# Kernel tuning notes

Measured on AMD Instinct MI355X. Metric: run time of the kernel, lower is better.

Reference implementation:

```python
import jax, jax.numpy as jnp
import numpy as np

B, S, D = 2, 2048, 1024
H, DQK, DV = 16, 64, 64
DECAY = 0.85


def _fractal_weights(seq_len: int, decay: float) -> np.ndarray:
    # Dragon-curve hierarchical weights: earlier (coarser) positions get higher
    # weight; weight decays by `decay` per hierarchy level. Normalized to sum 1,
    # matching DragonCurveGenerator.get_hierarchical_weights semantics.
    idx = np.arange(seq_len)
    level = np.floor(np.log2(idx + 1)).astype(np.int32)
    w = decay ** level.astype(np.float32)
    return (w / w.sum()).astype(np.float32)


def setup_inputs() -> dict:
    key = jax.random.key(0)
    kx, kq, kk, kv, ko = jax.random.split(key, 5)
    s = 1.0 / np.sqrt(D)
    return {
        "x": jax.random.normal(kx, (B, S, D), dtype=jnp.float32),
        "Wq": jax.random.normal(kq, (D, H * DQK), dtype=jnp.float32) * s,
        "Wk": jax.random.normal(kk, (D, H * DQK), dtype=jnp.float32) * s,
        "Wv": jax.random.normal(kv, (D, H * DV), dtype=jnp.float32) * s,
        "Wo": jax.random.normal(ko, (H * DV, D), dtype=jnp.float32) * s,
        "fractal_weights": jnp.asarray(_fractal_weights(S, DECAY)),
    }


def reference(x, Wq, Wk, Wv, Wo, fractal_weights):
    b, s, _ = x.shape
    # Projections (Linear with bias=False); weights stored as (in, out).
    Q = (x @ Wq).reshape(b, s, H, DQK).transpose(0, 2, 1, 3)  # [B,H,S,Dqk]
    K = (x @ Wk).reshape(b, s, H, DQK).transpose(0, 2, 1, 3)
    V = (x @ Wv).reshape(b, s, H, DV).transpose(0, 2, 1, 3)   # [B,H,S,Dv]
    scale = 1.0 / jnp.sqrt(jnp.asarray(DQK, dtype=x.dtype))
    scores = jnp.einsum("bhqd,bhkd->bhqk", Q, K) * scale      # [B,H,S,S]
    # Multiplicative per-key fractal bias applied BEFORE softmax.
    scores = scores * fractal_weights[None, None, None, :]
    attn = jax.nn.softmax(scores, axis=-1)
    out = jnp.einsum("bhqk,bhkd->bhqd", attn, V)               # [B,H,S,Dv]
    out = out.transpose(0, 2, 1, 3).reshape(b, s, H * DV)
    return out @ Wo                                            # [B,S,D]
```

## Files before the change

### kernel.cpp

```cpp
#include <hip/hip_runtime.h>
#include <hip/hip_bf16.h>
#include <stdint.h>

#define B_  2
#define S_  2048
#define D_  1024
#define H_  16
#define DH_ 64

typedef __attribute__((ext_vector_type(8))) __bf16    bf16x8;
typedef __attribute__((ext_vector_type(8))) _Float16  f16x8;
typedef __attribute__((ext_vector_type(4))) _Float16  f16x4;
typedef __attribute__((ext_vector_type(2))) __fp16    fp16x2;
typedef __attribute__((ext_vector_type(4))) float     f32x4;

__device__ inline unsigned short f2bf(float f) {
    union { float f; uint32_t u; } v; v.f = f;
    uint32_t r = (v.u + 0x7fffu + ((v.u >> 16) & 1u)) >> 16;
    return (unsigned short)r;
}

__device__ __forceinline__ void g2l16(const unsigned short* g, unsigned short* l) {
    __builtin_amdgcn_global_load_lds(
        (const __attribute__((address_space(1))) unsigned int*)g,
        (__attribute__((address_space(3))) unsigned int*)l,
        16, 0, 0);
}

__global__ void prep(const float* __restrict__ x, unsigned short* __restrict__ xb,
                     const float* __restrict__ s0, const float* __restrict__ s1,
                     const float* __restrict__ s2, const float* __restrict__ s3,
                     unsigned short* __restrict__ d0, unsigned short* __restrict__ d1,
                     unsigned short* __restrict__ d2, unsigned short* __restrict__ d3)
{
    __shared__ float tile[32][33];
    int bid = blockIdx.x, tid = threadIdx.x;
    if (bid < 4096) {
        int i = (bid * 256 + tid) * 4;
        float4 v = *(const float4*)(x + i);
        ushort4 o;
        o.x = f2bf(v.x); o.y = f2bf(v.y); o.z = f2bf(v.z); o.w = f2bf(v.w);
        *(ushort4*)(xb + i) = o;
    } else {
        int tb = bid - 4096;
        int z = tb >> 10, t = tb & 1023;
        int bx = t & 31, by = t >> 5;
        const float* src; unsigned short* dst;
        switch (z) {
            case 0: src = s0; dst = d0; break;
            case 1: src = s1; dst = d1; break;
            case 2: src = s2; dst = d2; break;
            default: src = s3; dst = d3; break;
        }
        int n0 = bx * 32, k0 = by * 32;
        int tx = tid & 31, ty = tid >> 5;
        for (int j = 0; j < 32; j += 8)
            tile[ty + j][tx] = src[(long)(k0 + ty + j) * 1024 + n0 + tx];
        __syncthreads();
        for (int j = 0; j < 32; j += 8)
            dst[(long)(n0 + ty + j) * 1024 + k0 + tx] = f2bf(tile[tx][ty + j]);
    }
}

__global__ __launch_bounds__(512, 4)
void gemm128(const unsigned short* __restrict__ A, const unsigned short* __restrict__ Bt,
             unsigned short* __restrict__ Qo, unsigned short* __restrict__ Ko,
             unsigned short* __restrict__ Vt,
             const float* __restrict__ fw)
{
    __shared__ __align__(16) unsigned short Smem[2][128 * 64];
    unsigned short* As = &Smem[0][0];
    unsigned short* Bs = &Smem[1][0];
    const int tid  = threadIdx.x;
    const int lane = tid & 63, wid = tid >> 6;
    const int quad = lane >> 4, l15 = lane & 15;
    const int ks   = wid >> 2;
    const int wm   = (wid >> 1) & 1, wn = wid & 1;
    const int lin = blockIdx.y * 24 + blockIdx.x;
    const int xcd = lin & 7, idx = lin >> 3;
    const int bn = (xcd & 1) * 12 + idx % 12;
    const int bm = (xcd >> 1) * 8 + idx / 12;
    const int K = 1024;
    f32x4 acc[4][4] = {};
    const long Abase = (long)bm * 128 * K;
    const long Bbase = (long)bn * 128 * K;

    for (int k0 = 0; k0 < K; k0 += 64) {
        __syncthreads();
#pragma unroll
        for (int i = 0; i < 2; i++) {
            int base = i * 512 + wid * 64;
            int slot = base + lane;
            int row = slot >> 3, cp = slot & 7;
            int c = cp ^ (row & 7);
            g2l16(A + Abase + (long)row * K + k0 + c * 8, &As[base * 8]);
        }
#pragma unroll
        for (int i = 0; i < 2; i++) {
            int base = i * 512 + wid * 64;
            int slot = base + lane;
            int row = slot >> 3, cp = slot & 7;
            int c = cp ^ (row & 7);
            g2l16(Bt + Bbase + (long)row * K + k0 + c * 8, &Bs[base * 8]);
        }
        __syncthreads();
        bf16x8 af[4], bfr[4];
#pragma unroll
        for (int t = 0; t < 4; t++) {
            int ra = wm * 64 + t * 16 + l15;
            af[t]  = *(const bf16x8*)(As + ra * 64 + (((ks * 4 + quad) ^ (l15 & 7))) * 8);
            int rb = wn * 64 + t * 16 + l15;
            bfr[t] = *(const bf16x8*)(Bs + rb * 64 + (((ks * 4 + quad) ^ (l15 & 7))) * 8);
        }
#pragma unroll
        for (int tm = 0; tm < 4; tm++)
#pragma unroll
            for (int tn = 0; tn < 4; tn++)
                acc[tm][tn] = __builtin_amdgcn_mfma_f32_16x16x32_bf16(af[tm], bfr[tn], acc[tm][tn], 0, 0, 0);
    }

    __syncthreads();

    float* ov = (float*)&Smem[0][0];
    const int slot = wm * 2 + wn;
    const float Cq = 0.125f * 1.44269504f;

#pragma unroll
    for (int p = 0; p < 4; p++) {
        if (ks == 1) {
#pragma unroll
            for (int tn = 0; tn < 4; tn++)
#pragma unroll
                for (int r = 0; r < 4; r++)
                    ov[((slot * 16) + quad * 4 + r) * 66 + tn * 16 + l15] = acc[p][tn][r];
        }
        __syncthreads();
        if (ks == 0) {
#pragma unroll
            for (int tn = 0; tn < 4; tn++)
#pragma unroll
                for (int r = 0; r < 4; r++) {
                    float v = acc[p][tn][r] + ov[((slot * 16) + quad * 4 + r) * 66 + tn * 16 + l15];
                    int gm = bm * 128 + wm * 64 + p * 16 + quad * 4 + r;
                    int gn = bn * 128 + wn * 64 + tn * 16 + l15;
                    int b = gm >> 11, s = gm & 2047;
                    if (gn < 1024) {
                        int h = gn >> 6, d = gn & 63;
                        Qo[(((long)(b * H_ + h) * S_ + s) << 6) + d] = f2bf(v * Cq);
                    } else if (gn < 2048) {
                        int g = gn - 1024; int h = g >> 6, d = g & 63;
                        Ko[(((long)(b * H_ + h) * S_ + s) << 6) + d] = f2bf(v * fw[s]);
                    } else {
                        int g = gn - 2048; int h = g >> 6, d = g & 63;
                        union { _Float16 h; unsigned short u; } cv;
                        cv.h = (_Float16)v;
                        int sp = s ^ ((d & 8) ? 4 : 0);
                        Vt[((long)(b * H_ + h) * DH_ + d) * S_ + sp] = cv.u;
                    }
                }
        }
        __syncthreads();
    }
}

__global__ __launch_bounds__(256, 4)
void gemm_wo(const unsigned short* __restrict__ A, const unsigned short* __restrict__ Bt,
             float* __restrict__ Cout)
{
    __shared__ __align__(16) unsigned short As[64 * 64];
    __shared__ __align__(16) unsigned short Bs[64 * 64];
    const int tid  = threadIdx.x;
    const int lane = tid & 63, wid = tid >> 6;
    const int quad = lane >> 4, l15 = lane & 15;
    const int lin = blockIdx.y * 16 + blockIdx.x;
    const int xcd = lin & 7, idx = lin >> 3;
    const int bn = (xcd & 1) * 8 + (idx & 7);
    const int bm = (xcd >> 1) * 16 + (idx >> 3);
    const int K = 1024;
    f32x4 acc[4] = {};
    const long Abase = (long)bm * 64 * K;
    const long Bbase = (long)bn * 64 * K;

    for (int k0 = 0; k0 < K; k0 += 64) {
        __syncthreads();
#pragma unroll
        for (int i = 0; i < 2; i++) {
            int base = i * 256 + wid * 64;
            int slot = base + lane;
            int row = slot >> 3, cp = slot & 7;
            int c = cp ^ (row & 7);
            g2l16(A + Abase + (long)row * K + k0 + c * 8, &As[base * 8]);
        }
#pragma unroll
        for (int i = 0; i < 2; i++) {
            int base = i * 256 + wid * 64;
            int slot = base + lane;
            int row = slot >> 3, cp = slot & 7;
            int c = cp ^ (row & 7);
            g2l16(Bt + Bbase + (long)row * K + k0 + c * 8, &Bs[base * 8]);
        }
        __syncthreads();
#pragma unroll
        for (int ks = 0; ks < 2; ks++) {
            bf16x8 af, bfr[4];
            {
                int ra = wid * 16 + l15;
                af = *(const bf16x8*)(As + ra * 64 + (((ks * 4 + quad) ^ (l15 & 7))) * 8);
            }
#pragma unroll
            for (int tt = 0; tt < 4; tt++) {
                int rb = tt * 16 + l15;
                bfr[tt] = *(const bf16x8*)(Bs + rb * 64 + (((ks * 4 + quad) ^ (l15 & 7))) * 8);
            }
#pragma unroll
            for (int tn = 0; tn < 4; tn++)
                acc[tn] = __builtin_amdgcn_mfma_f32_16x16x32_bf16(af, bfr[tn], acc[tn], 0, 0, 0);
        }
    }

    for (int tn = 0; tn < 4; tn++)
        for (int r = 0; r < 4; r++) {
            int gm = bm * 64 + wid * 16 + quad * 4 + r;
            int gn = bn * 64 + tn * 16 + l15;
            Cout[(long)gm * 1024 + gn] = acc[tn][r];
        }
}

__global__ __launch_bounds__(512, 2)
void attn_kernel(const unsigned short* __restrict__ Q, const unsigned short* __restrict__ Kb,
                 const unsigned short* __restrict__ Vt,
                 unsigned short* __restrict__ O)
{
    __shared__ __align__(16) unsigned short smem[2][2][2][64 * 64];

    const int tid  = threadIdx.x;
    const int lane = tid & 63, wid = tid >> 6;
    const int half = wid >> 2, sw = wid & 3;
    const int quad = lane >> 4, l15 = lane & 15;
    const int lin = blockIdx.y * 8 + blockIdx.x;
    const int xcd = lin & 7, idx = lin >> 3;
    const int bh = xcd * 4 + (idx & 3);
    const int qt = idx >> 2;

    const unsigned short* Kg = Kb + (long)bh * S_ * DH_;
    const unsigned short* Vg = Vt + (long)bh * (long)DH_ * S_;

    bf16x8 qf[4][2];
#pragma unroll
    for (int st = 0; st < 4; st++) {
        const unsigned short* Qp = Q + ((long)bh * S_ + qt * 256 + sw * 64 + st * 16 + l15) * DH_ + quad * 8;
        qf[st][0] = *(const bf16x8*)(Qp);
        qf[st][1] = *(const bf16x8*)(Qp + 32);
    }

    auto issue = [&](int buf, int kt) {
#pragma unroll
        for (int i = 0; i < 2; i++) {
            int base = i * 256 + sw * 64;
            int slot = base + lane;
            int row = slot >> 3, cp = slot & 7;
            int c = cp ^ (row & 7);
            g2l16(Kg + ((long)(kt * 64 + row) * 64 + c * 8), &smem[half][buf][0][base * 8]);
        }
#pragma unroll
        for (int i = 0; i < 2; i++) {
            int base = i * 256 + sw * 64;
            int slot = base + lane;
            int row = slot >> 3, cp = slot & 7;
            int c = cp ^ (row & 7);
            g2l16(Vg + ((long)row * S_ + kt * 64 + c * 8), &smem[half][buf][1][base * 8]);
        }
    };

    f32x4 oacc[4][4] = {};
    f32x4 lacc[4] = {};
    const f16x8 vone = {(_Float16)1.f, (_Float16)1.f, (_Float16)1.f, (_Float16)1.f,
                        (_Float16)1.f, (_Float16)1.f, (_Float16)1.f, (_Float16)1.f};

    const int kt0 = half * 16;
    issue(0, kt0);
    __syncthreads();

    const int hf = (((quad & 1) ^ ((l15 >> 3) & 1))) * 4;

    for (int t = 0; t < 16; t++) {
        const int cur = t & 1;
        if (t + 1 < 16) issue(1 - cur, kt0 + t + 1);

        const unsigned short* Kc = &smem[half][cur][0][0];
        const unsigned short* Vc = &smem[half][cur][1][0];

        f32x4 sacc[4][4] = {};
#pragma unroll
        for (int kc = 0; kc < 4; kc++) {
            int row = kc * 16 + l15;
            bf16x8 k0 = *(const bf16x8*)(Kc + (row * 8 + (quad       ^ (l15 & 7))) * 8);
            bf16x8 k1 = *(const bf16x8*)(Kc + (row * 8 + ((4 + quad) ^ (l15 & 7))) * 8);
#pragma unroll
            for (int st = 0; st < 4; st++) {
                sacc[st][kc] = __builtin_amdgcn_mfma_f32_16x16x32_bf16(k0, qf[st][0], sacc[st][kc], 0, 0, 0);
                sacc[st][kc] = __builtin_amdgcn_mfma_f32_16x16x32_bf16(k1, qf[st][1], sacc[st][kc], 0, 0, 0);
            }
        }

        f16x8 vfr[2][4];
#pragma unroll
        for (int c = 0; c < 2; c++)
#pragma unroll
            for (int dt = 0; dt < 4; dt++) {
                int row = dt * 16 + l15;
                int p0 = (c * 4 +     (quad >> 1)) ^ (l15 & 7);
                int p1 = (c * 4 + 2 + (quad >> 1)) ^ (l15 & 7);
                f16x4 v0 = *(const f16x4*)(Vc + row * 64 + p0 * 8 + hf);
                f16x4 v1 = *(const f16x4*)(Vc + row * 64 + p1 * 8 + hf);
                vfr[c][dt] = __builtin_shufflevector(v0, v1, 0, 1, 2, 3, 4, 5, 6, 7);
            }

        f16x8 pk8[4][2];
#pragma unroll
        for (int st = 0; st < 4; st++)
#pragma unroll
            for (int c = 0; c < 2; c++) {
                union { uint4 u; f16x8 v; } pku;
#pragma unroll
                for (int hh = 0; hh < 2; hh++) {
                    float p0 = __builtin_amdgcn_exp2f(sacc[st][2 * c + hh][0]);
                    float p1 = __builtin_amdgcn_exp2f(sacc[st][2 * c + hh][1]);
                    float p2 = __builtin_amdgcn_exp2f(sacc[st][2 * c + hh][2]);
                    float p3 = __builtin_amdgcn_exp2f(sacc[st][2 * c + hh][3]);
                    union { fp16x2 h2; unsigned int u; } a, b;
                    a.h2 = __builtin_amdgcn_cvt_pkrtz(p0, p1);
                    b.h2 = __builtin_amdgcn_cvt_pkrtz(p2, p3);
                    if (hh == 0) { pku.u.x = a.u; pku.u.y = b.u; }
                    else         { pku.u.z = a.u; pku.u.w = b.u; }
                }
                pk8[st][c] = pku.v;
            }

#pragma unroll
        for (int c = 0; c < 2; c++) {
#pragma unroll
            for (int st = 0; st < 4; st++)
                lacc[st] = __builtin_amdgcn_mfma_f32_16x16x32_f16(pk8[st][c], vone, lacc[st], 0, 0, 0);
#pragma unroll
            for (int dt = 0; dt < 4; dt++)
#pragma unroll
                for (int st = 0; st < 4; st++)
                    oacc[st][dt] = __builtin_amdgcn_mfma_f32_16x16x32_f16(pk8[st][c], vfr[c][dt], oacc[st][dt], 0, 0, 0);
        }

        __syncthreads();
    }

    float* ov = (float*)&smem[0][0][0][0];
    float* lv = ov + 128 * 66;
    int b = bh >> 4, h = bh & 15;

#pragma unroll
    for (int p = 0; p < 2; p++) {
        if (half == 1) {
#pragma unroll
            for (int si = 0; si < 2; si++) {
                int st = 2 * p + si;
#pragma unroll
                for (int dt = 0; dt < 4; dt++)
#pragma unroll
                    for (int r = 0; r < 4; r++) {
                        int qr = sw * 32 + si * 16 + quad * 4 + r;
                        ov[qr * 66 + dt * 16 + l15] = oacc[st][dt][r];
                    }
                if (l15 == 0) {
#pragma unroll
                    for (int r = 0; r < 4; r++)
                        lv[sw * 32 + si * 16 + quad * 4 + r] = lacc[st][r];
                }
            }
        }
        __syncthreads();
        if (half == 0) {
#pragma unroll
            for (int si = 0; si < 2; si++) {
                int st = 2 * p + si;
#pragma unroll
                for (int r = 0; r < 4; r++) {
                    int qr = sw * 32 + si * 16 + quad * 4 + r;
                    float inv = 1.0f / (lacc[st][r] + lv[qr]);
                    int srow = qt * 256 + sw * 64 + st * 16 + quad * 4 + r;
#pragma unroll
                    for (int dt = 0; dt < 4; dt++) {
                        float val = oacc[st][dt][r] + ov[qr * 66 + dt * 16 + l15];
                        O[((long)(b * S_ + srow)) * 1024 + h * DH_ + dt * 16 + l15] = f2bf(val * inv);
                    }
                }
            }
        }
        __syncthreads();
    }
}


extern "C" void kernel_launch(void* const* d_in, const int* in_sizes, int n_in,
                              void* d_out, int out_size, void* d_ws, size_t ws_size,
                              hipStream_t stream)
{
    const float* x  = (const float*)d_in[0];
    const float* Wq = (const float*)d_in[1];
    const float* Wk = (const float*)d_in[2];
    const float* Wv = (const float*)d_in[3];
    const float* Wo = (const float*)d_in[4];
    const float* fw = (const float*)d_in[5];
    float* out = (float*)d_out;

    char* ws = (char*)d_ws;
    unsigned short* xb    = (unsigned short*)(ws);
    unsigned short* WqkvT = (unsigned short*)(ws + 8388608);
    unsigned short* WoT   = (unsigned short*)(ws + 14680064);
    unsigned short* Qb    = (unsigned short*)(ws + 16777216);
    unsigned short* Kb    = (unsigned short*)(ws + 25165824);
    unsigned short* Vt    = (unsigned short*)(ws + 33554432);
    unsigned short* Ob    = xb;

    prep<<<dim3(4096 + 4096), dim3(256), 0, stream>>>(
        x, xb, Wq, Wk, Wv, Wo,
        WqkvT, WqkvT + 1024 * 1024, WqkvT + 2 * 1024 * 1024, WoT);
    gemm128<<<dim3(24, 32), dim3(512), 0, stream>>>(xb, WqkvT, Qb, Kb, Vt, fw);
    attn_kernel<<<dim3(S_ / 256, B_ * H_), dim3(512), 0, stream>>>(Qb, Kb, Vt, Ob);
    gemm_wo<<<dim3(16, 64), dim3(256), 0, stream>>>(Ob, WoT, out);
}
```

Measured before the change: 181.9 us.

## Retile QKV projection GEMM to 256x192 tiles with 16 waves, drop split-K reduction

The QKV projection GEMM moves from 128x128 tiles with a two-way split-K across 8 waves to 256x192 tiles computed by 16 waves, each owning a 64x48 sub-tile over the full K. This removes the shared-memory split-K reduction and its extra barriers in the epilogue, and raises data reuse per loaded tile. The grid shrinks from 768 to 256 blocks of 1024 threads, which is exactly one wave of blocks on 256 CUs but lowers occupancy and latency hiding per CU.

```diff
diff --git a/kernel.cpp b/kernel.cpp
--- a/kernel.cpp
+++ b/kernel.cpp
@@ -62,105 +62,96 @@
     }
 }
 
-__global__ __launch_bounds__(512, 4)
+__global__ __launch_bounds__(1024, 4)
 void gemm128(const unsigned short* __restrict__ A, const unsigned short* __restrict__ Bt,
              unsigned short* __restrict__ Qo, unsigned short* __restrict__ Ko,
              unsigned short* __restrict__ Vt,
              const float* __restrict__ fw)
 {
-    __shared__ __align__(16) unsigned short Smem[2][128 * 64];
-    unsigned short* As = &Smem[0][0];
-    unsigned short* Bs = &Smem[1][0];
+    __shared__ __align__(16) unsigned short As[256 * 64];
+    __shared__ __align__(16) unsigned short Bs[192 * 64];
     const int tid  = threadIdx.x;
     const int lane = tid & 63, wid = tid >> 6;
     const int quad = lane >> 4, l15 = lane & 15;
-    const int ks   = wid >> 2;
-    const int wm   = (wid >> 1) & 1, wn = wid & 1;
-    const int lin = blockIdx.y * 24 + blockIdx.x;
+    const int wr = wid >> 2, wc = wid & 3;
+    const int lin = blockIdx.y * 16 + blockIdx.x;
     const int xcd = lin & 7, idx = lin >> 3;
-    const int bn = (xcd & 1) * 12 + idx % 12;
-    const int bm = (xcd >> 1) * 8 + idx / 12;
+    const int bn = (xcd & 1) * 8 + (idx & 7);
+    const int bm = (xcd >> 1) * 4 + (idx >> 3);
     const int K = 1024;
-    f32x4 acc[4][4] = {};
-    const long Abase = (long)bm * 128 * K;
-    const long Bbase = (long)bn * 128 * K;
+    f32x4 acc[4][3] = {};
+    const long Abase = (long)bm * 256 * K;
+    const long Bbase = (long)bn * 192 * K;
 
     for (int k0 = 0; k0 < K; k0 += 64) {
         __syncthreads();
 #pragma unroll
         for (int i = 0; i < 2; i++) {
-            int base = i * 512 + wid * 64;
+            int base = i * 1024 + wid * 64;
             int slot = base + lane;
             int row = slot >> 3, cp = slot & 7;
             int c = cp ^ (row & 7);
             g2l16(A + Abase + (long)row * K + k0 + c * 8, &As[base * 8]);
         }
-#pragma unroll
-        for (int i = 0; i < 2; i++) {
-            int base = i * 512 + wid * 64;
+        {
+            int base = wid * 64;
             int slot = base + lane;
             int row = slot >> 3, cp = slot & 7;
             int c = cp ^ (row & 7);
             g2l16(Bt + Bbase + (long)row * K + k0 + c * 8, &Bs[base * 8]);
         }
-        __syncthreads();
-        bf16x8 af[4], bfr[4];
-#pragma unroll
-        for (int t = 0; t < 4; t++) {
-            int ra = wm * 64 + t * 16 + l15;
-            af[t]  = *(const bf16x8*)(As + ra * 64 + (((ks * 4 + quad) ^ (l15 & 7))) * 8);
-            int rb = wn * 64 + t * 16 + l15;
-            bfr[t] = *(const bf16x8*)(Bs + rb * 64 + (((ks * 4 + quad) ^ (l15 & 7))) * 8);
-        }
-#pragma unroll
-        for (int tm = 0; tm < 4; tm++)
-#pragma unroll
-            for (int tn = 0; tn < 4; tn++)
-                acc[tm][tn] = __builtin_amdgcn_mfma_f32_16x16x32_bf16(af[tm], bfr[tn], acc[tm][tn], 0, 0, 0);
-    }
-
-    __syncthreads();
-
-    float* ov = (float*)&Smem[0][0];
-    const int slot = wm * 2 + wn;
+        if (wid < 8) {
+            int base = 1024 + wid * 64;
+            int slot = base + lane;
+            int row = slot >> 3, cp = slot & 7;
+            int c = cp ^ (row & 7);
+            g2l16(Bt + Bbase + (long)row * K + k0 + c * 8, &Bs[base * 8]);
+        }
+        __syncthreads();
+#pragma unroll
+        for (int ks = 0; ks < 2; ks++) {
+            bf16x8 af[4], bfr[3];
+            int chunk = ((ks * 4 + quad) ^ (l15 & 7)) * 8;
+#pragma unroll
+            for (int t = 0; t < 4; t++) {
+                int ra = wr * 64 + t * 16 + l15;
+                af[t] = *(const bf16x8*)(As + ra * 64 + chunk);
+            }
+#pragma unroll
+            for (int u = 0; u < 3; u++) {
+                int rb = wc * 48 + u * 16 + l15;
+                bfr[u] = *(const bf16x8*)(Bs + rb * 64 + chunk);
+            }
+#pragma unroll
+            for (int tm = 0; tm < 4; tm++)
+#pragma unroll
+                for (int tn = 0; tn < 3; tn++)
+                    acc[tm][tn] = __builtin_amdgcn_mfma_f32_16x16x32_bf16(af[tm], bfr[tn], acc[tm][tn], 0, 0, 0);
+        }
+    }
+
     const float Cq = 0.125f * 1.44269504f;
-
-#pragma unroll
-    for (int p = 0; p < 4; p++) {
-        if (ks == 1) {
-#pragma unroll
-            for (int tn = 0; tn < 4; tn++)
-#pragma unroll
-                for (int r = 0; r < 4; r++)
-                    ov[((slot * 16) + quad * 4 + r) * 66 + tn * 16 + l15] = acc[p][tn][r];
-        }
-        __syncthreads();
-        if (ks == 0) {
-#pragma unroll
-            for (int tn = 0; tn < 4; tn++)
-#pragma unroll
-                for (int r = 0; r < 4; r++) {
-                    float v = acc[p][tn][r] + ov[((slot * 16) + quad * 4 + r) * 66 + tn * 16 + l15];
-                    int gm = bm * 128 + wm * 64 + p * 16 + quad * 4 + r;
-                    int gn = bn * 128 + wn * 64 + tn * 16 + l15;
-                    int b = gm >> 11, s = gm & 2047;
-                    if (gn < 1024) {
-                        int h = gn >> 6, d = gn & 63;
-                        Qo[(((long)(b * H_ + h) * S_ + s) << 6) + d] = f2bf(v * Cq);
-                    } else if (gn < 2048) {
-                        int g = gn - 1024; int h = g >> 6, d = g & 63;
-                        Ko[(((long)(b * H_ + h) * S_ + s) << 6) + d] = f2bf(v * fw[s]);
-                    } else {
-                        int g = gn - 2048; int h = g >> 6, d = g & 63;
-                        union { _Float16 h; unsigned short u; } cv;
-                        cv.h = (_Float16)v;
-                        int sp = s ^ ((d & 8) ? 4 : 0);
-                        Vt[((long)(b * H_ + h) * DH_ + d) * S_ + sp] = cv.u;
-                    }
+    for (int tm = 0; tm < 4; tm++)
+        for (int tn = 0; tn < 3; tn++)
+            for (int r = 0; r < 4; r++) {
+                int gm = bm * 256 + wr * 64 + tm * 16 + quad * 4 + r;
+                int gn = bn * 192 + wc * 48 + tn * 16 + l15;
+                float v = acc[tm][tn][r];
+                int b = gm >> 11, s = gm & 2047;
+                if (gn < 1024) {
+                    int h = gn >> 6, d = gn & 63;
+                    Qo[(((long)(b * H_ + h) * S_ + s) << 6) + d] = f2bf(v * Cq);
+                } else if (gn < 2048) {
+                    int g = gn - 1024; int h = g >> 6, d = g & 63;
+                    Ko[(((long)(b * H_ + h) * S_ + s) << 6) + d] = f2bf(v * fw[s]);
+                } else {
+                    int g = gn - 2048; int h = g >> 6, d = g & 63;
+                    union { _Float16 h; unsigned short u; } cv;
+                    cv.h = (_Float16)v;
+                    int sp = s ^ ((d & 8) ? 4 : 0);
+                    Vt[((long)(b * H_ + h) * DH_ + d) * S_ + sp] = cv.u;
                 }
-        }
-        __syncthreads();
-    }
+            }
 }
 
 __global__ __launch_bounds__(256, 4)
@@ -423,7 +414,7 @@
     prep<<<dim3(4096 + 4096), dim3(256), 0, stream>>>(
         x, xb, Wq, Wk, Wv, Wo,
         WqkvT, WqkvT + 1024 * 1024, WqkvT + 2 * 1024 * 1024, WoT);
-    gemm128<<<dim3(24, 32), dim3(512), 0, stream>>>(xb, WqkvT, Qb, Kb, Vt, fw);
+    gemm128<<<dim3(16, 16), dim3(1024), 0, stream>>>(xb, WqkvT, Qb, Kb, Vt, fw);
     attn_kernel<<<dim3(S_ / 256, B_ * H_), dim3(512), 0, stream>>>(Qb, Kb, Vt, Ob);
     gemm_wo<<<dim3(16, 64), dim3(256), 0, stream>>>(Ob, WoT, out);
 }
```

New measurement: 176.4 us. -3.0%, faster.
